# Optimization experiments

Measured on AMD Instinct MI355X. Metric: run time of the kernel, lower is better.

Reference implementation:

```python
import jax, jax.numpy as jnp
import numpy as np

B, T, DIM, H = 2, 2048, 1024, 16
HD = DIM // H


def setup_inputs() -> dict:
    key = jax.random.key(0)
    k1, k2, k3 = jax.random.split(key, 3)
    std = 1.0 / np.sqrt(DIM)
    x = jax.random.normal(k1, (B, T, DIM), dtype=jnp.float32)
    # torch Linear(dim, 3*dim).weight is [3*dim, dim]; we store the transposed
    # [dim, 3*dim] layout so forward is x @ W_qkv (same math).
    W_qkv = jax.random.uniform(k2, (DIM, 3 * DIM), dtype=jnp.float32, minval=-std, maxval=std)
    W_proj = jax.random.uniform(k3, (DIM, DIM), dtype=jnp.float32, minval=-std, maxval=std)
    return {"x": x, "W_qkv": W_qkv, "W_proj": W_proj}


def reference(x, W_qkv, W_proj):
    Bv, Tv, C = x.shape
    # qkv projection -> [B, T, 3, H, HD] -> q,k,v each [B, H, T, HD]
    qkv = (x @ W_qkv).reshape(Bv, Tv, 3, H, HD)
    qkv = jnp.transpose(qkv, (2, 0, 3, 1, 4))
    q, k, v = qkv[0], qkv[1], qkv[2]
    scale = jnp.asarray(np.sqrt(HD), dtype=x.dtype)
    scores = jnp.einsum('bhqd,bhkd->bhqk', q, k) / scale
    causal = jnp.tril(jnp.ones((Tv, Tv), dtype=bool))  # [T, T]
    scores = jnp.where(causal[None, None, :, :], scores, -jnp.inf)
    attn = jax.nn.softmax(scores, axis=-1)  # [B, H, T, T]
    # entropy per query position, averaged over heads -> [B, T]
    entropy = -(attn * jnp.log(attn + 1e-9)).sum(axis=-1).mean(axis=1)
    # dropout is identity in eval mode
    out = jnp.einsum('bhqk,bhkd->bhqd', attn, v)
    out = jnp.transpose(out, (0, 2, 1, 3)).reshape(Bv, Tv, C)
    return out @ W_proj, entropy
```

## Files before the change

kernel.cpp:

```cpp
#include <hip/hip_runtime.h>


typedef unsigned short u16;
typedef __attribute__((ext_vector_type(8))) __bf16 bf16x8;
typedef __attribute__((ext_vector_type(4))) float float4v;

#define BQ 2
#define TQ 2048
#define DIMQ 1024
#define HQ 16
#define HDQ 64

__device__ __forceinline__ float4v mfma16(bf16x8 a, bf16x8 b, float4v c) {
    return __builtin_amdgcn_mfma_f32_16x16x32_bf16(a, b, c, 0, 0, 0);
}

__device__ __forceinline__ u16 f2bf(float f) {
    unsigned x = __float_as_uint(f);
    return (u16)((x + 0x7FFFu + ((x >> 16) & 1u)) >> 16);
}

__device__ __forceinline__ uint4 cvt8(float4 a, float4 b) {
    union { uint4 v; u16 u[8]; } r;
    r.u[0] = f2bf(a.x); r.u[1] = f2bf(a.y); r.u[2] = f2bf(a.z); r.u[3] = f2bf(a.w);
    r.u[4] = f2bf(b.x); r.u[5] = f2bf(b.y); r.u[6] = f2bf(b.z); r.u[7] = f2bf(b.w);
    return r.v;
}

__device__ __forceinline__ void async16(const u16* g, u16* l) {
    __builtin_amdgcn_global_load_lds(
        (const __attribute__((address_space(1))) void*)g,
        (__attribute__((address_space(3))) void*)l, 16, 0, 0);
}

__device__ __forceinline__ void plswap(unsigned& a, unsigned& b) {
    asm("v_permlane32_swap_b32 %0, %1" : "+v"(a), "+v"(b));
    asm("v_permlane16_swap_b32 %0, %1" : "+v"(a), "+v"(b));
}

__device__ __forceinline__ void tr_tile(
    const float* __restrict__ in, u16* __restrict__ out, int R, int C,
    int tx, int ty, int tid, float (*T)[68])
{
    const int k0 = ty * 64, n0 = tx * 64;
    {
        int r = tid >> 2, cc = (tid & 3) << 4;
        const float* src = in + (size_t)(k0 + r) * C + n0 + cc;
        float4 v0 = ((const float4*)src)[0];
        float4 v1 = ((const float4*)src)[1];
        float4 v2 = ((const float4*)src)[2];
        float4 v3 = ((const float4*)src)[3];
        *(float4*)&T[r][cc + 0]  = v0;
        *(float4*)&T[r][cc + 4]  = v1;
        *(float4*)&T[r][cc + 8]  = v2;
        *(float4*)&T[r][cc + 12] = v3;
    }
    __syncthreads();
    {
        int nr = tid >> 2, kc = (tid & 3) << 4;
        union { uint4 v; u16 u[8]; } o0, o1;
#pragma unroll
        for (int j = 0; j < 8; ++j) o0.u[j] = f2bf(T[kc + j][nr]);
#pragma unroll
        for (int j = 0; j < 8; ++j) o1.u[j] = f2bf(T[kc + 8 + j][nr]);
        u16* dst = out + (size_t)(n0 + nr) * R + k0 + kc;
        ((uint4*)dst)[0] = o0.v;
        *(uint4*)(dst + 8) = o1.v;
    }
}

__global__ __launch_bounds__(256) void prep_kernel(
    const float* __restrict__ x, const float* __restrict__ Wq,
    const float* __restrict__ Wp,
    u16* __restrict__ xb, u16* __restrict__ Wt, u16* __restrict__ Wpt)
{
    __shared__ float T[64][68];
    const int bx = blockIdx.x, tid = threadIdx.x;
    if (bx < 2048) {
        int i = (bx * 256 + tid) * 8;
        float4 a = *(const float4*)(x + i);
        float4 b = *(const float4*)(x + i + 4);
        *(uint4*)(xb + i) = cvt8(a, b);
    } else if (bx < 2816) {
        int bb = bx - 2048;
        tr_tile(Wq, Wt, DIMQ, 3 * DIMQ, bb % 48, bb / 48, tid, T);
    } else {
        int bb = bx - 2816;
        tr_tile(Wp, Wpt, DIMQ, DIMQ, bb & 15, bb >> 4, tid, T);
    }
}

__global__ __launch_bounds__(256) void tr_cvt(
    const float* __restrict__ in, u16* __restrict__ out, int R, int C)
{
    __shared__ float T[64][68];
    tr_tile(in, out, R, C, blockIdx.x, blockIdx.y, threadIdx.x, T);
}

template <int TILEM, int MODE>
__global__ __launch_bounds__(256) void gemm_db(
    const u16* __restrict__ A, const u16* __restrict__ Bt,
    int M, int N, int K,
    u16* __restrict__ Qo, u16* __restrict__ Ko, u16* __restrict__ Vt,
    float* __restrict__ Of, const float* __restrict__ EntIn)
{
    constexpr int MT = TILEM / 32;
    constexpr int AR = TILEM / 64;
    __shared__ u16 As[2][TILEM * 32];
    __shared__ u16 Bs[2][128 * 32];

    const int tid = threadIdx.x;
    const int nbn = gridDim.x;
    const int flat = blockIdx.y * nbn + blockIdx.x;
    const int cpx = (nbn * gridDim.y) >> 3;
    const int swz = (flat & 7) * cpx + (flat >> 3);
    const int bm = swz / nbn, bn = swz % nbn;
    const int wave = tid >> 6, lane = tid & 63;
    const int quad = lane >> 4, c = lane & 15;
    const int wm = wave >> 1, wn = wave & 1;
    const int x3 = c & 3;

    const float4v z = {0.f, 0.f, 0.f, 0.f};
    float4v acc[MT][4];
#pragma unroll
    for (int mt = 0; mt < MT; ++mt)
#pragma unroll
        for (int tn = 0; tn < 4; ++tn) acc[mt][tn] = z;

    const int srow = tid >> 2;
    const int schunk8 = (((tid & 3) ^ (srow & 3)) << 3);
    const u16* ga = A  + (size_t)(bm * TILEM + srow) * K + schunk8;
    const u16* gb = Bt + (size_t)(bn * 128  + srow) * K + schunk8;

#pragma unroll
    for (int p = 0; p < AR; ++p)
        async16(ga + (size_t)(p * 64) * K, As[0] + p * 2048 + tid * 8);
#pragma unroll
    for (int p = 0; p < 2; ++p)
        async16(gb + (size_t)(p * 64) * K, Bs[0] + p * 2048 + tid * 8);

    const int niter = K >> 5;
    for (int it = 0; it < niter; ++it) {
        __syncthreads();
        if (it + 1 < niter) {
            const int nb = (it + 1) & 1;
            const int kc = (it + 1) * 32;
#pragma unroll
            for (int p = 0; p < AR; ++p)
                async16(ga + kc + (size_t)(p * 64) * K, As[nb] + p * 2048 + tid * 8);
#pragma unroll
            for (int p = 0; p < 2; ++p)
                async16(gb + kc + (size_t)(p * 64) * K, Bs[nb] + p * 2048 + tid * 8);
        }
        const u16* as = As[it & 1];
        const u16* bs = Bs[it & 1];

        bf16x8 af[MT], bfr[4];
#pragma unroll
        for (int mt = 0; mt < MT; ++mt)
            af[mt] = *(const bf16x8*)&as[(wm * (TILEM / 2) + mt * 16 + c) * 32 +
                                         ((quad ^ x3) << 3)];
#pragma unroll
        for (int tn = 0; tn < 4; ++tn)
            bfr[tn] = *(const bf16x8*)&bs[(wn * 64 + tn * 16 + c) * 32 +
                                          ((quad ^ x3) << 3)];
#pragma unroll
        for (int mt = 0; mt < MT; ++mt)
#pragma unroll
            for (int tn = 0; tn < 4; ++tn)
                acc[mt][tn] = mfma16(af[mt], bfr[tn], acc[mt][tn]);
    }

#pragma unroll
    for (int mt = 0; mt < MT; ++mt)
#pragma unroll
        for (int tn = 0; tn < 4; ++tn) {
            int gm0 = bm * TILEM + wm * (TILEM / 2) + mt * 16 + quad * 4;
            int gn  = bn * 128 + wn * 64 + tn * 16 + c;
            if (MODE == 0) {
                int s = gn >> 10, h = (gn >> 6) & 15, d = gn & 63;
                int b = gm0 >> 11, t0 = gm0 & 2047;
                size_t bh = (size_t)(b * HQ + h);
                if (s == 2) {
                    union { unsigned long long w; u16 u[4]; } pk;
#pragma unroll
                    for (int r = 0; r < 4; ++r) pk.u[r] = f2bf(acc[mt][tn][r]);
                    *(unsigned long long*)&Vt[(bh * HDQ + d) * TQ + t0] = pk.w;
                } else {
                    u16* dst = (s == 0) ? Qo : Ko;
                    float sc = (s == 0) ? 0.18033688f : 1.0f;
#pragma unroll
                    for (int r = 0; r < 4; ++r)
                        dst[(bh * TQ + t0 + r) * HDQ + d] = f2bf(acc[mt][tn][r] * sc);
                }
            } else {
#pragma unroll
                for (int r = 0; r < 4; ++r)
                    Of[(size_t)(gm0 + r) * N + gn] = acc[mt][tn][r];
            }
        }

    if (MODE == 1 && bn == 0 && bm < 16) {
        int i = bm * 256 + tid;
        int b = i >> 11, t = i & 2047;
        float s = 0.f;
#pragma unroll
        for (int h = 0; h < HQ; ++h) s += EntIn[((size_t)(b * HQ + h)) * TQ + t];
        Of[(size_t)BQ * TQ * DIMQ + i] = s * (1.0f / HQ);
    }
}

__global__ __launch_bounds__(256) void attn_kernel(
    const u16* __restrict__ Q, const u16* __restrict__ K,
    const u16* __restrict__ Vt, u16* __restrict__ AO,
    float* __restrict__ Ent)
{
    const int d = blockIdx.x;
    const int j = d >> 3;
    const int bh = (d & 7) * 4 + (j >> 4);
    int pt = j & 15;
    if (j & 32) pt = 15 - pt;
    const int qt1 = pt;
    const int qt2 = 31 - pt;

    const int tid = threadIdx.x;
    const int wave = tid >> 6, lane = tid & 63;
    const int quad = lane >> 4, c = lane & 15;
    const int x7 = c & 7;

    __shared__ u16 Ks[2][64 * 64];
    __shared__ u16 Vs[2][64 * 64];

    const u16* Qp = Q  + (size_t)bh * TQ * HDQ;
    const u16* Kp = K  + (size_t)bh * TQ * HDQ;
    const u16* Vp = Vt + (size_t)bh * HDQ * TQ;

    const int q0[2] = { qt1 * 64 + wave * 16, qt2 * 64 + wave * 16 };

    bf16x8 qf[2][2];
#pragma unroll
    for (int s = 0; s < 2; ++s) {
        const u16* qr = Qp + (size_t)(q0[s] + c) * HDQ;
        qf[s][0] = *(const bf16x8*)(qr + quad * 8);
        qf[s][1] = *(const bf16x8*)(qr + 32 + quad * 8);
    }

    const float MX2 = 17.312336f;
    const float4v z = {0.f, 0.f, 0.f, 0.f};
    const float4v mz = {-MX2, -MX2, -MX2, -MX2};
    float4v oacc[2][4];
#pragma unroll
    for (int s = 0; s < 2; ++s)
#pragma unroll
        for (int tn = 0; tn < 4; ++tn) oacc[s][tn] = z;
    float lp4[2][4] = {{0.f,0.f,0.f,0.f},{0.f,0.f,0.f,0.f}};
    float tp4[2][4] = {{0.f,0.f,0.f,0.f},{0.f,0.f,0.f,0.f}};

    const int ntile = qt2 + 1;

    const int srow = tid >> 3;
    const int schunk8 = (((tid & 7) ^ (srow & 7)) << 3);
    const u16* ka = Kp + (size_t)srow * HDQ + schunk8;
    const u16* va = Vp + (size_t)srow * TQ + schunk8;

    {
        async16(ka, Ks[0] + tid * 8);
        async16(ka + (size_t)32 * HDQ, Ks[0] + 2048 + tid * 8);
        async16(va, Vs[0] + tid * 8);
        async16(va + (size_t)32 * TQ, Vs[0] + 2048 + tid * 8);
    }

    for (int jt = 0; jt < ntile; ++jt) {
        __syncthreads();
        if (jt + 1 < ntile) {
            int nb = (jt + 1) & 1;
            async16(ka + (size_t)((jt + 1) * 64) * HDQ, Ks[nb] + tid * 8);
            async16(ka + (size_t)((jt + 1) * 64 + 32) * HDQ, Ks[nb] + 2048 + tid * 8);
            async16(va + (jt + 1) * 64, Vs[nb] + tid * 8);
            async16(va + (size_t)32 * TQ + (jt + 1) * 64, Vs[nb] + 2048 + tid * 8);
        }
        const u16* ksb = Ks[jt & 1];
        const u16* vsb = Vs[jt & 1];

        bf16x8 kf[4][2], vf[4][2];
#pragma unroll
        for (int tn = 0; tn < 4; ++tn) {
            int base = (tn * 16 + c) * 64;
            kf[tn][0] = *(const bf16x8*)&ksb[base + ((quad ^ x7) << 3)];
            kf[tn][1] = *(const bf16x8*)&ksb[base + (((quad + 4) ^ x7) << 3)];
            vf[tn][0] = *(const bf16x8*)&vsb[base + ((quad ^ x7) << 3)];
            vf[tn][1] = *(const bf16x8*)&vsb[base + (((quad + 4) ^ x7) << 3)];
        }

#pragma unroll
        for (int s = 0; s < 2; ++s) {
            if (s == 0 && jt > qt1) continue;
            const int diag = s ? qt2 : qt1;
            unsigned w0[4], w1[4];
#pragma unroll
            for (int tn = 0; tn < 4; ++tn) {
                float4v sacc = mz;
                __builtin_amdgcn_s_setprio(1);
                sacc = mfma16(kf[tn][0], qf[s][0], sacc);
                sacc = mfma16(kf[tn][1], qf[s][1], sacc);
                __builtin_amdgcn_s_setprio(0);
                if (jt == diag) {
#pragma unroll
                    for (int r = 0; r < 4; ++r) {
                        int kg = jt * 64 + tn * 16 + quad * 4 + r;
                        if (kg > q0[s] + c) sacc[r] = -1e30f;
                    }
                }
                float pv[4];
#pragma unroll
                for (int r = 0; r < 4; ++r) {
                    float sv = sacc[r];
                    float p;
                    asm("v_exp_f32 %0, %1" : "=v"(p) : "v"(sv));
                    lp4[s][r] += p;
                    tp4[s][r] += p * sv;
                    pv[r] = p;
                }
                asm("v_cvt_pk_bf16_f32 %0, %1, %2"
                    : "=v"(w0[tn]) : "v"(pv[0]), "v"(pv[1]));
                asm("v_cvt_pk_bf16_f32 %0, %1, %2"
                    : "=v"(w1[tn]) : "v"(pv[2]), "v"(pv[3]));
            }
            plswap(w0[0], w0[1]);
            plswap(w1[0], w1[1]);
            plswap(w0[2], w0[3]);
            plswap(w1[2], w1[3]);
            union { uint4 u; bf16x8 v; } P0, P1;
            P0.u = (uint4){w0[0], w1[0], w0[1], w1[1]};
            P1.u = (uint4){w0[2], w1[2], w0[3], w1[3]};
            __builtin_amdgcn_s_setprio(1);
#pragma unroll
            for (int tn = 0; tn < 4; ++tn) {
                oacc[s][tn] = mfma16(vf[tn][0], P0.v, oacc[s][tn]);
                oacc[s][tn] = mfma16(vf[tn][1], P1.v, oacc[s][tn]);
            }
            __builtin_amdgcn_s_setprio(0);
        }
    }

    const int b = bh >> 4, h = bh & 15;
#pragma unroll
    for (int s = 0; s < 2; ++s) {
        float lp = (lp4[s][0] + lp4[s][1]) + (lp4[s][2] + lp4[s][3]);
        float tp = (tp4[s][0] + tp4[s][1]) + (tp4[s][2] + tp4[s][3]);
        lp += __shfl_xor(lp, 16); lp += __shfl_xor(lp, 32);
        tp += __shfl_xor(tp, 16); tp += __shfl_xor(tp, 32);

        float inv = 1.0f / lp;
        u16* dst = AO + ((size_t)(b * TQ + q0[s] + c)) * DIMQ + h * HDQ;
#pragma unroll
        for (int tn = 0; tn < 4; ++tn) {
            unsigned u[4];
#pragma unroll
            for (int r = 0; r < 4; ++r)
                u[r] = (unsigned)f2bf(oacc[s][tn][r] * inv);
            uint2 pk;
            pk.x = u[0] | (u[1] << 16);
            pk.y = u[2] | (u[3] << 16);
            *(uint2*)(dst + tn * 16 + quad * 4) = pk;
        }
        if (quad == 0)
            Ent[(size_t)bh * TQ + q0[s] + c] =
                __logf(lp) - 0.69314718f * tp / lp;
    }
}

extern "C" void kernel_launch(void* const* d_in, const int* in_sizes, int n_in,
                              void* d_out, int out_size, void* d_ws, size_t ws_size,
                              hipStream_t stream) {
    const float* x     = (const float*)d_in[0];
    const float* Wqkv  = (const float*)d_in[1];
    const float* Wproj = (const float*)d_in[2];
    float* out = (float*)d_out;

    const size_t NE = (size_t)BQ * HQ * TQ * HDQ;
    const size_t WQN = (size_t)3 * DIMQ * DIMQ;
    const size_t WPN = (size_t)DIMQ * DIMQ;
    u16* Qb  = (u16*)d_ws;
    u16* Kb  = Qb + NE;
    u16* Vtb = Kb + NE;
    u16* xb  = Vtb + NE;
    u16* Wt  = xb + NE;
    u16* AO  = xb;

    const size_t need = (4 * NE + WQN + WPN) * 2 + (size_t)BQ * HQ * TQ * 4;
    const bool room = ws_size >= need;
    u16* Wpt = room ? (Wt + WQN) : Wt;
    float* Ent = room ? (float*)(Wpt + WPN) : (float*)(Wt + WQN);

    prep_kernel<<<dim3(room ? 3072 : 2816), 256, 0, stream>>>(
        x, Wqkv, Wproj, xb, Wt, Wpt);
    gemm_db<128, 0><<<dim3(24, 32), 256, 0, stream>>>(
        xb, Wt, BQ * TQ, 3 * DIMQ, DIMQ, Qb, Kb, Vtb, nullptr, nullptr);
    if (!room)
        tr_cvt<<<dim3(16, 16), 256, 0, stream>>>(Wproj, Wpt, DIMQ, DIMQ);
    attn_kernel<<<dim3(512), 256, 0, stream>>>(Qb, Kb, Vtb, AO, Ent);
    gemm_db<64, 1><<<dim3(8, 64), 256, 0, stream>>>(
        AO, Wpt, BQ * TQ, DIMQ, DIMQ, nullptr, nullptr, nullptr, out, Ent);
}
```

Baseline: 176.3 us.

## Split attention query tiles across 8 waves with 512-thread blocks

The attention kernel moves from 256 threads, where each wave handled both paired query tiles, to 512 threads, where waves 0-3 own the first query tile and waves 4-7 own the mirrored second tile. Each thread now issues half as many K/V async copies, holds one set of accumulators instead of two, and collapses the per-row partial sums into scalars. It also drops the setprio around the QK MFMAs. The aim is lower register pressure and more waves to hide latency. The cost is that the first-tile waves sit idle after their causal range while still waiting at every barrier, and the larger blocks may reduce how many blocks fit per CU.

```diff
diff --git a/kernel.cpp b/kernel.cpp
--- a/kernel.cpp
+++ b/kernel.cpp
@@ -210,7 +210,7 @@
     }
 }
 
-__global__ __launch_bounds__(256) void attn_kernel(
+__global__ __launch_bounds__(512) void attn_kernel(
     const u16* __restrict__ Q, const u16* __restrict__ K,
     const u16* __restrict__ Vt, u16* __restrict__ AO,
     float* __restrict__ Ent)
@@ -225,6 +225,8 @@
 
     const int tid = threadIdx.x;
     const int wave = tid >> 6, lane = tid & 63;
+    const int sw = wave >> 2;
+    const int wq = wave & 3;
     const int quad = lane >> 4, c = lane & 15;
     const int x7 = c & 7;
 
@@ -235,26 +237,23 @@
     const u16* Kp = K  + (size_t)bh * TQ * HDQ;
     const u16* Vp = Vt + (size_t)bh * HDQ * TQ;
 
-    const int q0[2] = { qt1 * 64 + wave * 16, qt2 * 64 + wave * 16 };
-
-    bf16x8 qf[2][2];
-#pragma unroll
-    for (int s = 0; s < 2; ++s) {
-        const u16* qr = Qp + (size_t)(q0[s] + c) * HDQ;
-        qf[s][0] = *(const bf16x8*)(qr + quad * 8);
-        qf[s][1] = *(const bf16x8*)(qr + 32 + quad * 8);
+    const int qt_mine = sw ? qt2 : qt1;
+    const int q0 = qt_mine * 64 + wq * 16;
+
+    bf16x8 qf[2];
+    {
+        const u16* qr = Qp + (size_t)(q0 + c) * HDQ;
+        qf[0] = *(const bf16x8*)(qr + quad * 8);
+        qf[1] = *(const bf16x8*)(qr + 32 + quad * 8);
     }
 
     const float MX2 = 17.312336f;
     const float4v z = {0.f, 0.f, 0.f, 0.f};
     const float4v mz = {-MX2, -MX2, -MX2, -MX2};
-    float4v oacc[2][4];
-#pragma unroll
-    for (int s = 0; s < 2; ++s)
-#pragma unroll
-        for (int tn = 0; tn < 4; ++tn) oacc[s][tn] = z;
-    float lp4[2][4] = {{0.f,0.f,0.f,0.f},{0.f,0.f,0.f,0.f}};
-    float tp4[2][4] = {{0.f,0.f,0.f,0.f},{0.f,0.f,0.f,0.f}};
+    float4v oacc[4];
+#pragma unroll
+    for (int tn = 0; tn < 4; ++tn) oacc[tn] = z;
+    float lp = 0.f, tp = 0.f;
 
     const int ntile = qt2 + 1;
 
@@ -265,9 +264,7 @@
 
     {
         async16(ka, Ks[0] + tid * 8);
-        async16(ka + (size_t)32 * HDQ, Ks[0] + 2048 + tid * 8);
         async16(va, Vs[0] + tid * 8);
-        async16(va + (size_t)32 * TQ, Vs[0] + 2048 + tid * 8);
     }
 
     for (int jt = 0; jt < ntile; ++jt) {
@@ -275,40 +272,34 @@
         if (jt + 1 < ntile) {
             int nb = (jt + 1) & 1;
             async16(ka + (size_t)((jt + 1) * 64) * HDQ, Ks[nb] + tid * 8);
-            async16(ka + (size_t)((jt + 1) * 64 + 32) * HDQ, Ks[nb] + 2048 + tid * 8);
             async16(va + (jt + 1) * 64, Vs[nb] + tid * 8);
-            async16(va + (size_t)32 * TQ + (jt + 1) * 64, Vs[nb] + 2048 + tid * 8);
-        }
-        const u16* ksb = Ks[jt & 1];
-        const u16* vsb = Vs[jt & 1];
-
-        bf16x8 kf[4][2], vf[4][2];
-#pragma unroll
-        for (int tn = 0; tn < 4; ++tn) {
-            int base = (tn * 16 + c) * 64;
-            kf[tn][0] = *(const bf16x8*)&ksb[base + ((quad ^ x7) << 3)];
-            kf[tn][1] = *(const bf16x8*)&ksb[base + (((quad + 4) ^ x7) << 3)];
-            vf[tn][0] = *(const bf16x8*)&vsb[base + ((quad ^ x7) << 3)];
-            vf[tn][1] = *(const bf16x8*)&vsb[base + (((quad + 4) ^ x7) << 3)];
-        }
-
-#pragma unroll
-        for (int s = 0; s < 2; ++s) {
-            if (s == 0 && jt > qt1) continue;
-            const int diag = s ? qt2 : qt1;
+        }
+
+        if (sw == 1 || jt <= qt1) {
+            const u16* ksb = Ks[jt & 1];
+            const u16* vsb = Vs[jt & 1];
+
+            bf16x8 kf[4][2], vf[4][2];
+#pragma unroll
+            for (int tn = 0; tn < 4; ++tn) {
+                int base = (tn * 16 + c) * 64;
+                kf[tn][0] = *(const bf16x8*)&ksb[base + ((quad ^ x7) << 3)];
+                kf[tn][1] = *(const bf16x8*)&ksb[base + (((quad + 4) ^ x7) << 3)];
+                vf[tn][0] = *(const bf16x8*)&vsb[base + ((quad ^ x7) << 3)];
+                vf[tn][1] = *(const bf16x8*)&vsb[base + (((quad + 4) ^ x7) << 3)];
+            }
+
             unsigned w0[4], w1[4];
 #pragma unroll
             for (int tn = 0; tn < 4; ++tn) {
                 float4v sacc = mz;
-                __builtin_amdgcn_s_setprio(1);
-                sacc = mfma16(kf[tn][0], qf[s][0], sacc);
-                sacc = mfma16(kf[tn][1], qf[s][1], sacc);
-                __builtin_amdgcn_s_setprio(0);
-                if (jt == diag) {
+                sacc = mfma16(kf[tn][0], qf[0], sacc);
+                sacc = mfma16(kf[tn][1], qf[1], sacc);
+                if (jt == qt_mine) {
 #pragma unroll
                     for (int r = 0; r < 4; ++r) {
                         int kg = jt * 64 + tn * 16 + quad * 4 + r;
-                        if (kg > q0[s] + c) sacc[r] = -1e30f;
+                        if (kg > q0 + c) sacc[r] = -1e30f;
                     }
                 }
                 float pv[4];
@@ -317,8 +308,8 @@
                     float sv = sacc[r];
                     float p;
                     asm("v_exp_f32 %0, %1" : "=v"(p) : "v"(sv));
-                    lp4[s][r] += p;
-                    tp4[s][r] += p * sv;
+                    lp += p;
+                    tp += p * sv;
                     pv[r] = p;
                 }
                 asm("v_cvt_pk_bf16_f32 %0, %1, %2"
@@ -336,36 +327,33 @@
             __builtin_amdgcn_s_setprio(1);
 #pragma unroll
             for (int tn = 0; tn < 4; ++tn) {
-                oacc[s][tn] = mfma16(vf[tn][0], P0.v, oacc[s][tn]);
-                oacc[s][tn] = mfma16(vf[tn][1], P1.v, oacc[s][tn]);
+                oacc[tn] = mfma16(vf[tn][0], P0.v, oacc[tn]);
+                oacc[tn] = mfma16(vf[tn][1], P1.v, oacc[tn]);
             }
             __builtin_amdgcn_s_setprio(0);
         }
     }
 
+    lp += __shfl_xor(lp, 16); lp += __shfl_xor(lp, 32);
+    tp += __shfl_xor(tp, 16); tp += __shfl_xor(tp, 32);
+
     const int b = bh >> 4, h = bh & 15;
-#pragma unroll
-    for (int s = 0; s < 2; ++s) {
-        float lp = (lp4[s][0] + lp4[s][1]) + (lp4[s][2] + lp4[s][3]);
-        float tp = (tp4[s][0] + tp4[s][1]) + (tp4[s][2] + tp4[s][3]);
-        lp += __shfl_xor(lp, 16); lp += __shfl_xor(lp, 32);
-        tp += __shfl_xor(tp, 16); tp += __shfl_xor(tp, 32);
-
+    {
         float inv = 1.0f / lp;
-        u16* dst = AO + ((size_t)(b * TQ + q0[s] + c)) * DIMQ + h * HDQ;
+        u16* dst = AO + ((size_t)(b * TQ + q0 + c)) * DIMQ + h * HDQ;
 #pragma unroll
         for (int tn = 0; tn < 4; ++tn) {
             unsigned u[4];
 #pragma unroll
             for (int r = 0; r < 4; ++r)
-                u[r] = (unsigned)f2bf(oacc[s][tn][r] * inv);
+                u[r] = (unsigned)f2bf(oacc[tn][r] * inv);
             uint2 pk;
             pk.x = u[0] | (u[1] << 16);
             pk.y = u[2] | (u[3] << 16);
             *(uint2*)(dst + tn * 16 + quad * 4) = pk;
         }
         if (quad == 0)
-            Ent[(size_t)bh * TQ + q0[s] + c] =
+            Ent[(size_t)bh * TQ + q0 + c] =
                 __logf(lp) - 0.69314718f * tp / lp;
     }
 }
@@ -399,7 +387,7 @@
         xb, Wt, BQ * TQ, 3 * DIMQ, DIMQ, Qb, Kb, Vtb, nullptr, nullptr);
     if (!room)
         tr_cvt<<<dim3(16, 16), 256, 0, stream>>>(Wproj, Wpt, DIMQ, DIMQ);
-    attn_kernel<<<dim3(512), 256, 0, stream>>>(Qb, Kb, Vtb, AO, Ent);
+    attn_kernel<<<dim3(512), 512, 0, stream>>>(Qb, Kb, Vtb, AO, Ent);
     gemm_db<64, 1><<<dim3(8, 64), 256, 0, stream>>>(
         AO, Wpt, BQ * TQ, DIMQ, DIMQ, nullptr, nullptr, nullptr, out, Ent);
 }
```

Result: slower. 197.7 us (+12.2%).

## Process four query tiles per attention block to reuse K/V tiles

Applied to the files above, without the earlier changes.

Each attention block now handles four query tiles (balanced pairs from both ends of the causal range) instead of two, halving the grid to 256 blocks. Every K/V tile loaded into shared memory now feeds up to four query tiles, cutting K/V traffic and load overhead. The change also drops the setprio hints and collapses the per-row partial sums into single accumulators, which lengthens the serial dependency chain. In exchange, register pressure rises (four Q fragments and sixteen accumulators) and fewer blocks are available to fill the 256 CUs.

```diff
diff --git a/kernel.cpp b/kernel.cpp
--- a/kernel.cpp
+++ b/kernel.cpp
@@ -217,11 +217,9 @@
 {
     const int d = blockIdx.x;
     const int j = d >> 3;
-    const int bh = (d & 7) * 4 + (j >> 4);
-    int pt = j & 15;
-    if (j & 32) pt = 15 - pt;
-    const int qt1 = pt;
-    const int qt2 = 31 - pt;
+    const int bh = (d & 7) * 4 + (j >> 3);
+    const int ptg = j & 7;
+    const int qt[4] = { ptg, 8 + ptg, 23 - ptg, 31 - ptg };
 
     const int tid = threadIdx.x;
     const int wave = tid >> 6, lane = tid & 63;
@@ -235,11 +233,13 @@
     const u16* Kp = K  + (size_t)bh * TQ * HDQ;
     const u16* Vp = Vt + (size_t)bh * HDQ * TQ;
 
-    const int q0[2] = { qt1 * 64 + wave * 16, qt2 * 64 + wave * 16 };
-
-    bf16x8 qf[2][2];
-#pragma unroll
-    for (int s = 0; s < 2; ++s) {
+    int q0[4];
+#pragma unroll
+    for (int s = 0; s < 4; ++s) q0[s] = qt[s] * 64 + wave * 16;
+
+    bf16x8 qf[4][2];
+#pragma unroll
+    for (int s = 0; s < 4; ++s) {
         const u16* qr = Qp + (size_t)(q0[s] + c) * HDQ;
         qf[s][0] = *(const bf16x8*)(qr + quad * 8);
         qf[s][1] = *(const bf16x8*)(qr + 32 + quad * 8);
@@ -248,15 +248,14 @@
     const float MX2 = 17.312336f;
     const float4v z = {0.f, 0.f, 0.f, 0.f};
     const float4v mz = {-MX2, -MX2, -MX2, -MX2};
-    float4v oacc[2][4];
-#pragma unroll
-    for (int s = 0; s < 2; ++s)
+    float4v oacc[4][4];
+#pragma unroll
+    for (int s = 0; s < 4; ++s)
 #pragma unroll
         for (int tn = 0; tn < 4; ++tn) oacc[s][tn] = z;
-    float lp4[2][4] = {{0.f,0.f,0.f,0.f},{0.f,0.f,0.f,0.f}};
-    float tp4[2][4] = {{0.f,0.f,0.f,0.f},{0.f,0.f,0.f,0.f}};
-
-    const int ntile = qt2 + 1;
+    float lp[4] = {0.f, 0.f, 0.f, 0.f}, tp[4] = {0.f, 0.f, 0.f, 0.f};
+
+    const int ntile = qt[3] + 1;
 
     const int srow = tid >> 3;
     const int schunk8 = (((tid & 7) ^ (srow & 7)) << 3);
@@ -293,18 +292,15 @@
         }
 
 #pragma unroll
-        for (int s = 0; s < 2; ++s) {
-            if (s == 0 && jt > qt1) continue;
-            const int diag = s ? qt2 : qt1;
+        for (int s = 0; s < 4; ++s) {
+            if (s < 3 && jt > qt[s]) continue;
             unsigned w0[4], w1[4];
 #pragma unroll
             for (int tn = 0; tn < 4; ++tn) {
                 float4v sacc = mz;
-                __builtin_amdgcn_s_setprio(1);
                 sacc = mfma16(kf[tn][0], qf[s][0], sacc);
                 sacc = mfma16(kf[tn][1], qf[s][1], sacc);
-                __builtin_amdgcn_s_setprio(0);
-                if (jt == diag) {
+                if (jt == qt[s]) {
 #pragma unroll
                     for (int r = 0; r < 4; ++r) {
                         int kg = jt * 64 + tn * 16 + quad * 4 + r;
@@ -317,8 +313,8 @@
                     float sv = sacc[r];
                     float p;
                     asm("v_exp_f32 %0, %1" : "=v"(p) : "v"(sv));
-                    lp4[s][r] += p;
-                    tp4[s][r] += p * sv;
+                    lp[s] += p;
+                    tp[s] += p * sv;
                     pv[r] = p;
                 }
                 asm("v_cvt_pk_bf16_f32 %0, %1, %2"
@@ -345,13 +341,12 @@
 
     const int b = bh >> 4, h = bh & 15;
 #pragma unroll
-    for (int s = 0; s < 2; ++s) {
-        float lp = (lp4[s][0] + lp4[s][1]) + (lp4[s][2] + lp4[s][3]);
-        float tp = (tp4[s][0] + tp4[s][1]) + (tp4[s][2] + tp4[s][3]);
-        lp += __shfl_xor(lp, 16); lp += __shfl_xor(lp, 32);
-        tp += __shfl_xor(tp, 16); tp += __shfl_xor(tp, 32);
-
-        float inv = 1.0f / lp;
+    for (int s = 0; s < 4; ++s) {
+        float l = lp[s], t = tp[s];
+        l += __shfl_xor(l, 16); l += __shfl_xor(l, 32);
+        t += __shfl_xor(t, 16); t += __shfl_xor(t, 32);
+
+        float inv = 1.0f / l;
         u16* dst = AO + ((size_t)(b * TQ + q0[s] + c)) * DIMQ + h * HDQ;
 #pragma unroll
         for (int tn = 0; tn < 4; ++tn) {
@@ -366,7 +361,7 @@
         }
         if (quad == 0)
             Ent[(size_t)bh * TQ + q0[s] + c] =
-                __logf(lp) - 0.69314718f * tp / lp;
+                __logf(l) - 0.69314718f * t / l;
     }
 }
 
@@ -399,7 +394,7 @@
         xb, Wt, BQ * TQ, 3 * DIMQ, DIMQ, Qb, Kb, Vtb, nullptr, nullptr);
     if (!room)
         tr_cvt<<<dim3(16, 16), 256, 0, stream>>>(Wproj, Wpt, DIMQ, DIMQ);
-    attn_kernel<<<dim3(512), 256, 0, stream>>>(Qb, Kb, Vtb, AO, Ent);
+    attn_kernel<<<dim3(256), 256, 0, stream>>>(Qb, Kb, Vtb, AO, Ent);
     gemm_db<64, 1><<<dim3(8, 64), 256, 0, stream>>>(
         AO, Wpt, BQ * TQ, DIMQ, DIMQ, nullptr, nullptr, nullptr, out, Ent);
 }
```

After: 182.8 us. 1.04x slower.
